# Performance work log

Hardware: AMD Instinct MI355X
Metric: run time of the kernel (lower is better)

The kernel has to match this reference:

```python
import jax, jax.numpy as jnp
import numpy as np
from jax import lax


def setup_inputs() -> dict:
    key = jax.random.key(0)
    ks = jax.random.split(key, 16)
    B, H, W, C = 4, 48, 48, 512
    N = H * W
    std = 0.02  # trunc_normal std in the torch init

    def nrm(k, shape, s=std):
        return jax.random.normal(k, shape, dtype=jnp.float32) * s

    return {
        "x": jax.random.normal(ks[0], (B, N, C), jnp.float32),
        "context": jax.random.normal(ks[1], (B, N, C), jnp.float32),
        "mask1": jax.random.uniform(ks[2], (B, N), jnp.float32),
        "mask2": jax.random.uniform(ks[3], (B, N), jnp.float32),
        "q_w": nrm(ks[4], (C, C)), "q_b": jnp.zeros((C,), jnp.float32),
        "kv1_w": nrm(ks[5], (C, C)), "kv1_b": jnp.zeros((C,), jnp.float32),
        "kv2_w": nrm(ks[6], (C, C)), "kv2_b": jnp.zeros((C,), jnp.float32),
        "f1_w": nrm(ks[7], (1, 48)), "f1_b": jnp.zeros((1,), jnp.float32),
        "f2_w": nrm(ks[8], (1, 12)), "f2_b": jnp.zeros((1,), jnp.float32),
        "lepe_w": nrm(ks[9], (C, C)), "lepe_b": jnp.zeros((C,), jnp.float32),
        "lepe_conv_w": nrm(ks[10], (C, 1, 3, 3), float(np.sqrt(2.0 / 9.0))),
        "lepe_conv_b": jnp.zeros((C,), jnp.float32),
        "proj_w": nrm(ks[11], (C, C)), "proj_b": jnp.zeros((C,), jnp.float32),
        "H": H, "W": W,
    }


def _lin(t, w, b):
    # torch nn.Linear: y = t @ W^T + b, W:[out,in]
    return t @ w.T + b


def _pooled_seq(ctx, idx, f1_w, f1_b, f2_w, f2_b):
    # ctx:[B,HW,C], idx:[B,HW] mask-sorted indices. sr_ratio==4 => groups of 48/12/1.
    B, HW, Cc = ctx.shape
    t1, t2 = HW // 192, HW // 24  # token1=(HW//48)//4, token2=(HW//12)//2
    g = jnp.take_along_axis(ctx, idx[:, :, None], axis=1)  # [B,HW,C] gathered
    p1 = g[:, : HW // 4].transpose(0, 2, 1).reshape(B, Cc, t1, 48)
    p2 = g[:, HW // 4 : 3 * HW // 4].transpose(0, 2, 1).reshape(B, Cc, t2, 12)
    p3 = g[:, 3 * HW // 4 :].transpose(0, 2, 1)  # [B,C,HW//4]
    a1 = (p1 @ f1_w.T)[..., 0] + f1_b  # [B,C,t1]
    a2 = (p2 @ f2_w.T)[..., 0] + f2_b  # [B,C,t2]
    return jnp.concatenate([a1, a2, p3], axis=-1).transpose(0, 2, 1)  # [B,Lkv,C]


def reference(x, context, mask1, mask2, q_w, q_b, kv1_w, kv1_b, kv2_w, kv2_b,
              f1_w, f1_b, f2_w, f2_b, lepe_w, lepe_b, lepe_conv_w, lepe_conv_b,
              proj_w, proj_b, H, W):
    B, N, C = x.shape
    nh = 8
    hd = C // nh
    scale = hd ** -0.5

    # lepe: linear + depthwise 3x3 conv positional encoding
    le = _lin(x, lepe_w, lepe_b).transpose(0, 2, 1).reshape(B, C, H, W)
    le = lax.conv_general_dilated(le, lepe_conv_w, (1, 1), ((1, 1), (1, 1)),
                                  dimension_numbers=("NCHW", "OIHW", "NCHW"),
                                  feature_group_count=C)
    lepe = (le + lepe_conv_b[None, :, None, None]).reshape(B, C, N).transpose(0, 2, 1)

    # mask-sorted grouped pooling of context (two orderings: row-major and transposed)
    idx1 = jnp.argsort(mask1, axis=1)
    idx2 = jnp.argsort(mask2, axis=1)
    ctx_t = context.reshape(B, H, W, C).transpose(0, 2, 1, 3).reshape(B, N, C)
    seq1 = _pooled_seq(context, idx1, f1_w, f1_b, f2_w, f2_b)
    seq2 = _pooled_seq(ctx_t, idx2, f1_w, f1_b, f2_w, f2_b)

    q = _lin(x, q_w, q_b).reshape(B, N, nh, hd).transpose(0, 2, 1, 3)  # [B,h,N,hd]
    kv1 = _lin(seq1, kv1_w, kv1_b).reshape(B, -1, 2, nh // 2, hd).transpose(2, 0, 3, 1, 4)
    kv2 = _lin(seq2, kv2_w, kv2_b).reshape(B, -1, 2, nh // 2, hd).transpose(2, 0, 3, 1, 4)
    k = jnp.concatenate([kv1[0], kv2[0]], axis=1)  # [B,h,Lkv,hd]
    v = jnp.concatenate([kv1[1], kv2[1]], axis=1)

    attn = jax.nn.softmax(jnp.einsum("bhnd,bhld->bhnl", q, k) * scale, axis=-1)
    out = jnp.einsum("bhnl,bhld->bhnd", attn, v).transpose(0, 2, 1, 3).reshape(B, N, C)
    return _lin(out + lepe, proj_w, proj_b)
```

## Files before the change

### kernel.cpp

```cpp
#include <hip/hip_runtime.h>
#include <hip/hip_bf16.h>
#include <math.h>

#define B_    4
#define H_    48
#define W_    48
#define N_    2304
#define C_    512
#define NH_   8
#define HD_   64
#define LKV_  684
#define LKP_  704

typedef __attribute__((ext_vector_type(8))) short short8;
typedef __attribute__((ext_vector_type(8))) unsigned short ushort8;
typedef __attribute__((ext_vector_type(4))) float f32x4;

#define MFMA16(a, b, c) __builtin_amdgcn_mfma_f32_16x16x32_bf16(a, b, c, 0, 0, 0)

__device__ __forceinline__ unsigned short f2bf(float f) {
  __hip_bfloat16 h = __float2bfloat16(f);
  return *reinterpret_cast<unsigned short*>(&h);
}
__device__ __forceinline__ float bf2f(unsigned short u) {
  unsigned int x = ((unsigned int)u) << 16;
  return *reinterpret_cast<float*>(&x);
}
__device__ __forceinline__ unsigned int cvtpk(float lo, float hi) {
  unsigned int r;
  asm("v_cvt_pk_bf16_f32 %0, %1, %2" : "=v"(r) : "v"(lo), "v"(hi));
  return r;
}
__device__ __forceinline__ void gld16(const unsigned short* g, unsigned short* l) {
  __builtin_amdgcn_global_load_lds(
      (const __attribute__((address_space(1))) void*)g,
      (__attribute__((address_space(3))) void*)l, 16, 0, 0);
}

#define SORTB 288
#define PACKB 1472

__global__ __launch_bounds__(256) void pack_sort(
    const float* __restrict__ lepe_w, const float* __restrict__ q_w,
    const float* __restrict__ kv1_w, const float* __restrict__ kv2_w,
    const float* __restrict__ proj_w, const float* __restrict__ x,
    unsigned short* __restrict__ wb, unsigned short* __restrict__ xb,
    const float* __restrict__ m1, const float* __restrict__ m2,
    int* __restrict__ i1, int* __restrict__ i2)
{
  __shared__ float key[N_];
  if (blockIdx.x >= SORTB) {
    int i = ((blockIdx.x - SORTB) * 256 + threadIdx.x) * 16;
    const float* s; unsigned short* d; int rel;
    if      (i < 262144)  { s = lepe_w; d = wb;           rel = i; }
    else if (i < 524288)  { s = q_w;    d = wb + 262144;  rel = i - 262144; }
    else if (i < 786432)  { s = kv1_w;  d = wb + 524288;  rel = i - 524288; }
    else if (i < 1048576) { s = kv2_w;  d = wb + 786432;  rel = i - 786432; }
    else if (i < 1310720) { s = proj_w; d = wb + 1048576; rel = i - 1048576; }
    else                  { s = x;      d = xb;           rel = i - 1310720; }
    const float4* sp = (const float4*)(s + rel);
    float4 v0 = sp[0], v1 = sp[1], v2 = sp[2], v3 = sp[3];
    ushort8 o0, o1;
    o0[0] = f2bf(v0.x); o0[1] = f2bf(v0.y); o0[2] = f2bf(v0.z); o0[3] = f2bf(v0.w);
    o0[4] = f2bf(v1.x); o0[5] = f2bf(v1.y); o0[6] = f2bf(v1.z); o0[7] = f2bf(v1.w);
    o1[0] = f2bf(v2.x); o1[1] = f2bf(v2.y); o1[2] = f2bf(v2.z); o1[3] = f2bf(v2.w);
    o1[4] = f2bf(v3.x); o1[5] = f2bf(v3.y); o1[6] = f2bf(v3.z); o1[7] = f2bf(v3.w);
    *(ushort8*)(d + rel)     = o0;
    *(ushort8*)(d + rel + 8) = o1;
    return;
  }
  const int blk = blockIdx.x;
  const int row = blk / 36, chunk = blk % 36;
  const float* m = (row < 4) ? (m1 + (size_t)row * N_) : (m2 + (size_t)(row - 4) * N_);
  int* out = (row < 4) ? (i1 + (size_t)row * N_) : (i2 + (size_t)(row - 4) * N_);
  for (int i = threadIdx.x; i < N_ / 4; i += 256)
    ((float4*)key)[i] = ((const float4*)m)[i];
  __syncthreads();
  const int e = chunk * 64 + (threadIdx.x >> 2);
  const int sl = threadIdx.x & 3;
  const float ki = key[e];
  int rank = 0;
  #pragma unroll 4
  for (int t = 0; t < N_ / 16; ++t) {
    int jb = sl * 4 + t * 16;
    float4 kv = *(const float4*)&key[jb];
    rank += (kv.x < ki) || (kv.x == ki && jb     < e);
    rank += (kv.y < ki) || (kv.y == ki && jb + 1 < e);
    rank += (kv.z < ki) || (kv.z == ki && jb + 2 < e);
    rank += (kv.w < ki) || (kv.w == ki && jb + 3 < e);
  }
  rank += __shfl_xor(rank, 1);
  rank += __shfl_xor(rank, 2);
  if (sl == 0) out[rank] = e;
}

struct GQuad {
  const unsigned short *A[4], *Bw[4];
  const float *bias[4];
  void *out[4];
  float sc[4];
  int bf[4];
  int nx[4];
  int cum[3];
};

__global__ __launch_bounds__(256) void gemm4(GQuad q, int K, int Nn)
{
  int id = blockIdx.x, cfg;
  if      (id < q.cum[0]) { cfg = 0; }
  else if (id < q.cum[1]) { cfg = 1; id -= q.cum[0]; }
  else if (id < q.cum[2]) { cfg = 2; id -= q.cum[1]; }
  else                    { cfg = 3; id -= q.cum[2]; }
  const int bx = id % q.nx[cfg], by = id / q.nx[cfg];

  const unsigned short* A  = q.A[cfg];
  const unsigned short* Bw = q.Bw[cfg];
  const float* bias        = q.bias[cfg];
  void* out                = q.out[cfg];
  const int out_bf16       = q.bf[cfg];
  const float oscale       = q.sc[cfg];

  __shared__ unsigned short Abuf[128 * 32];
  __shared__ unsigned short Bbuf[128 * 32];
  const int tid = threadIdx.x;
  const int l = tid & 63, w = tid >> 6;
  const int wm = w >> 1, wn = w & 1;
  const int lo16 = l & 15, hi = l >> 4;
  const int row0 = bx * 128, col0 = by * 128;
  const int srow = tid >> 2, scol = (tid & 3) * 8;

  const unsigned short* Asrc = A + (size_t)(row0 + srow) * K + scol;
  const unsigned short* Bsrc = Bw + (size_t)(col0 + srow) * K + scol;

  f32x4 acc[4][4];
  #pragma unroll
  for (int m = 0; m < 4; ++m)
    #pragma unroll
    for (int n = 0; n < 4; ++n)
      #pragma unroll
      for (int r = 0; r < 4; ++r) acc[m][n][r] = 0.f;

  for (int k0 = 0; k0 < K; k0 += 32) {
    __syncthreads();
    gld16(Asrc + k0,                   &Abuf[tid * 8]);
    gld16(Asrc + (size_t)64 * K + k0,  &Abuf[2048 + tid * 8]);
    gld16(Bsrc + k0,                   &Bbuf[tid * 8]);
    gld16(Bsrc + (size_t)64 * K + k0,  &Bbuf[2048 + tid * 8]);
    __syncthreads();
    short8 af[4], bf[4];
    #pragma unroll
    for (int m = 0; m < 4; ++m)
      af[m] = *(const short8*)&Abuf[(wm * 64 + m * 16 + lo16) * 32 + hi * 8];
    #pragma unroll
    for (int n = 0; n < 4; ++n)
      bf[n] = *(const short8*)&Bbuf[(wn * 64 + n * 16 + lo16) * 32 + hi * 8];
    #pragma unroll
    for (int m = 0; m < 4; ++m)
      #pragma unroll
      for (int n = 0; n < 4; ++n)
        acc[m][n] = MFMA16(af[m], bf[n], acc[m][n]);
  }

  #pragma unroll
  for (int m = 0; m < 4; ++m) {
    #pragma unroll
    for (int n = 0; n < 4; ++n) {
      int gcol = col0 + wn * 64 + n * 16 + lo16;
      #pragma unroll
      for (int r = 0; r < 4; ++r) {
        int grow = row0 + wm * 64 + m * 16 + hi * 4 + r;
        float v = acc[m][n][r] + bias[gcol];
        if (out_bf16)
          ((unsigned short*)out)[(size_t)grow * Nn + gcol] = f2bf(v * oscale);
        else
          ((float*)out)[(size_t)grow * Nn + gcol] = v;
      }
    }
  }
}

__global__ __launch_bounds__(256) void packconv(
    const unsigned short* __restrict__ kv1, const unsigned short* __restrict__ kv2,
    unsigned short* __restrict__ Kf, unsigned short* __restrict__ Vf,
    const unsigned short* __restrict__ lin, const float* __restrict__ cw,
    const float* __restrict__ cb, unsigned short* __restrict__ outp)
{
  __shared__ unsigned short Vt[64][72];
  const int tid = threadIdx.x;
  if (blockIdx.x < 352) {
    const int kb = blockIdx.x;
    const int bh = kb / 11, t = kb % 11;
    const int h = bh & 7, b = bh >> 3;
    const unsigned short* src = (h < 4) ? kv1 : kv2;
    const int hcol = (h & 3) * 64;

    #pragma unroll
    for (int pass = 0; pass < 2; ++pass) {
      int r = pass * 32 + (tid >> 3);
      int cc = (tid & 7) * 8;
      int l = t * 64 + r;
      uint4 v = make_uint4(0, 0, 0, 0);
      if (l < LKV_)
        v = *(const uint4*)&src[(size_t)(b * LKP_ + l) * C_ + 256 + hcol + cc];
      *(uint4*)&Vt[r][cc] = v;
    }
    __syncthreads();

    #pragma unroll
    for (int pass = 0; pass < 2; ++pass) {
      int o = pass * 256 + tid;
      int lane = o & 63, ns = o >> 6;
      int frag = ns >> 1, s = ns & 1;
      int lo16 = lane & 15, hi8 = (lane >> 4) * 8;
      size_t oidx = ((size_t)kb * 8 + ns) * 512 + lane * 8;
      {
        int l = t * 64 + frag * 16 + lo16;
        uint4 val = make_uint4(0, 0, 0, 0);
        if (l < LKV_)
          val = *(const uint4*)&src[(size_t)(b * LKP_ + l) * C_ + hcol + s * 32 + hi8];
        *(uint4*)&Kf[oidx] = val;
      }
      {
        unsigned short tmp[8];
        #pragma unroll
        for (int j = 0; j < 8; ++j)
          tmp[j] = Vt[s * 32 + hi8 + j][frag * 16 + lo16];
        *(uint4*)&Vf[oidx] = *(uint4*)tmp;
      }
    }
    return;
  }
  const int cg = tid & 63;
  const int wslot = (blockIdx.x - 352) * 4 + (tid >> 6);
  const int nslots = (gridDim.x - 352) * 4;

  float wf[72];
  const float* wsrc = cw + cg * 72;
  #pragma unroll
  for (int i = 0; i < 18; ++i)
    *(float4*)&wf[i * 4] = *(const float4*)(wsrc + i * 4);
  float bias[8];
  *(float4*)&bias[0] = *(const float4*)(cb + cg * 8);
  *(float4*)&bias[4] = *(const float4*)(cb + cg * 8 + 4);

  for (int pos = wslot; pos < B_ * N_; pos += nslots) {
    int wv = pos % W_;
    int r  = pos / W_;
    int hv = r % H_;
    int b  = r / H_;
    float acc[8];
    #pragma unroll
    for (int j = 0; j < 8; ++j) acc[j] = bias[j];
    #pragma unroll
    for (int dy = 0; dy < 3; ++dy) {
      int hh = hv + dy - 1;
      if (hh < 0 || hh >= H_) continue;
      #pragma unroll
      for (int dx = 0; dx < 3; ++dx) {
        int ww = wv + dx - 1;
        if (ww < 0 || ww >= W_) continue;
        ushort8 v = *(const ushort8*)(lin + ((((size_t)b * H_ + hh) * W_ + ww) * 64 + cg) * 8);
        #pragma unroll
        for (int j = 0; j < 8; ++j)
          acc[j] += wf[j * 9 + dy * 3 + dx] * bf2f(v[j]);
      }
    }
    ushort8 ov;
    #pragma unroll
    for (int j = 0; j < 8; ++j) ov[j] = f2bf(acc[j]);
    *(ushort8*)(outp + ((size_t)pos * 64 + cg) * 8) = ov;
  }
}

__global__ __launch_bounds__(256) void pool_kernel(
    const float* __restrict__ ctx,
    const int* __restrict__ idx1, const int* __restrict__ idx2,
    const float* __restrict__ f1w, const float* __restrict__ f1b,
    const float* __restrict__ f2w, const float* __restrict__ f2b_,
    unsigned short* __restrict__ seqb1, unsigned short* __restrict__ seqb2)
{
  int bl = blockIdx.x;
  const int transposed = bl >= B_ * LKP_;
  if (transposed) bl -= B_ * LKP_;
  const int* idx = transposed ? idx2 : idx1;
  unsigned short* seqb = transposed ? seqb2 : seqb1;
  int b = bl / LKP_, l = bl % LKP_;
  unsigned short* dst = seqb + ((size_t)b * LKP_ + l) * C_;
  int c0 = threadIdx.x, c1 = threadIdx.x + 256;
  if (l >= LKV_) { dst[c0] = 0; dst[c1] = 0; return; }
  const int* id = idx + (size_t)b * N_;
  int j0, cnt;
  const float* fw; float fb;
  if (l < 12)       { j0 = l * 48;              cnt = 48; fw = f1w; fb = f1b[0]; }
  else if (l < 108) { j0 = 576 + (l - 12) * 12; cnt = 12; fw = f2w; fb = f2b_[0]; }
  else              { j0 = 1728 + (l - 108);    cnt = 1;  fw = nullptr; fb = 0.f; }
  const float* cb = ctx + (size_t)b * N_ * C_;
  float a0 = fb, a1 = fb;
  int r = 0;
  for (; r + 4 <= cnt; r += 4) {
    int4 nv = *(const int4*)(id + j0 + r);
    int n0 = nv.x, n1 = nv.y, n2 = nv.z, n3 = nv.w;
    if (transposed) {
      n0 = (n0 % 48) * 48 + n0 / 48; n1 = (n1 % 48) * 48 + n1 / 48;
      n2 = (n2 % 48) * 48 + n2 / 48; n3 = (n3 % 48) * 48 + n3 / 48;
    }
    const float* s0 = cb + (size_t)n0 * C_;
    const float* s1 = cb + (size_t)n1 * C_;
    const float* s2 = cb + (size_t)n2 * C_;
    const float* s3 = cb + (size_t)n3 * C_;
    float w0 = fw[r], w1 = fw[r+1], w2 = fw[r+2], w3 = fw[r+3];
    a0 += w0 * s0[c0] + w1 * s1[c0] + w2 * s2[c0] + w3 * s3[c0];
    a1 += w0 * s0[c1] + w1 * s1[c1] + w2 * s2[c1] + w3 * s3[c1];
  }
  for (; r < cnt; ++r) {
    int n = id[j0 + r];
    if (transposed) n = (n % 48) * 48 + n / 48;
    const float* src = cb + (size_t)n * C_;
    float wr = fw ? fw[r] : 1.f;
    a0 += wr * src[c0];
    a1 += wr * src[c1];
  }
  dst[c0] = f2bf(a0);
  dst[c1] = f2bf(a1);
}

__global__ __launch_bounds__(256) void attn_kernel(
    const unsigned short* __restrict__ Qb, const unsigned short* __restrict__ Kf,
    const unsigned short* __restrict__ Vf, const unsigned short* __restrict__ lepe,
    unsigned short* __restrict__ outb)
{
  __shared__ unsigned short P[4][16][72];
  const int tid = threadIdx.x;
  const int l = tid & 63, wv = tid >> 6;
  const int lo16 = l & 15, hi = l >> 4;
  const int qt64 = blockIdx.x % (N_ / 64);
  const int bh = blockIdx.x / (N_ / 64);
  const int h = bh & 7, b = bh >> 3;
  const int qrow0 = qt64 * 64 + wv * 16;

  const unsigned short* qptr = Qb + ((size_t)b * N_ + qrow0 + lo16) * C_ + h * 64;
  short8 qf0 = *(const short8*)(qptr + hi * 8);
  short8 qf1 = *(const short8*)(qptr + 32 + hi * 8);

  const unsigned short* kbase = Kf + (size_t)bh * 11 * 4096 + (size_t)l * 8;
  const unsigned short* vbase = Vf + (size_t)bh * 11 * 4096 + (size_t)l * 8;

  float lsum = 0.f;
  f32x4 o[4];
  #pragma unroll
  for (int df = 0; df < 4; ++df)
    #pragma unroll
    for (int r = 0; r < 4; ++r) o[df][r] = 0.f;

  short8 ka0[4], ka1[4], kn0[4], kn1[4];
  #pragma unroll
  for (int n = 0; n < 4; ++n) {
    ka0[n] = *(const short8*)(kbase + (size_t)(n * 2 + 0) * 512);
    ka1[n] = *(const short8*)(kbase + (size_t)(n * 2 + 1) * 512);
  }

  for (int t = 0; t < 11; ++t) {
    short8 vf0[4], vf1[4];
    #pragma unroll
    for (int i = 0; i < 4; ++i) {
      vf0[i] = *(const short8*)(vbase + (size_t)(t * 8 + i * 2 + 0) * 512);
      vf1[i] = *(const short8*)(vbase + (size_t)(t * 8 + i * 2 + 1) * 512);
    }
    if (t < 10) {
      #pragma unroll
      for (int n = 0; n < 4; ++n) {
        kn0[n] = *(const short8*)(kbase + (size_t)((t + 1) * 8 + n * 2 + 0) * 512);
        kn1[n] = *(const short8*)(kbase + (size_t)((t + 1) * 8 + n * 2 + 1) * 512);
      }
    }
    const f32x4 z = {0.f, 0.f, 0.f, 0.f};
    f32x4 s[4];
    #pragma unroll
    for (int n = 0; n < 4; ++n) {
      s[n] = MFMA16(ka0[n], qf0, z);
      s[n] = MFMA16(ka1[n], qf1, s[n]);
    }
    if (t == 10) {
      #pragma unroll
      for (int n = 0; n < 4; ++n)
        #pragma unroll
        for (int r = 0; r < 4; ++r)
          if (n * 16 + hi * 4 + r >= LKV_ - 640) s[n][r] = -1e30f;
    }
    float psl = 0.f;
    #pragma unroll
    for (int n = 0; n < 4; ++n) {
      #pragma unroll
      for (int rp = 0; rp < 2; ++rp) {
        float e0 = exp2f(s[n][2 * rp]     - 8.f);
        float e1 = exp2f(s[n][2 * rp + 1] - 8.f);
        psl += e0 + e1;
        *(unsigned int*)&P[wv][lo16][n * 16 + hi * 4 + 2 * rp] = cvtpk(e0, e1);
      }
    }
    lsum += psl;
    short8 pa0 = *(const short8*)&P[wv][lo16][hi * 8];
    short8 pa1 = *(const short8*)&P[wv][lo16][32 + hi * 8];
    #pragma unroll
    for (int df = 0; df < 4; ++df) {
      o[df] = MFMA16(pa0, vf0[df], o[df]);
      o[df] = MFMA16(pa1, vf1[df], o[df]);
    }
    #pragma unroll
    for (int n = 0; n < 4; ++n) { ka0[n] = kn0[n]; ka1[n] = kn1[n]; }
  }

  lsum += __shfl_xor(lsum, 16);
  lsum += __shfl_xor(lsum, 32);
  float rr[4];
  #pragma unroll
  for (int r = 0; r < 4; ++r) rr[r] = 1.f / __shfl(lsum, hi * 4 + r);
  #pragma unroll
  for (int df = 0; df < 4; ++df)
    #pragma unroll
    for (int r = 0; r < 4; ++r) {
      size_t off = ((size_t)b * N_ + qrow0 + hi * 4 + r) * C_ + h * 64 + df * 16 + lo16;
      outb[off] = f2bf(o[df][r] * rr[r] + bf2f(lepe[off]));
    }
}

extern "C" void kernel_launch(void* const* d_in, const int* in_sizes, int n_in,
                              void* d_out, int out_size, void* d_ws, size_t ws_size,
                              hipStream_t stream)
{
  const float* x      = (const float*)d_in[0];
  const float* ctx    = (const float*)d_in[1];
  const float* mask1  = (const float*)d_in[2];
  const float* mask2  = (const float*)d_in[3];
  const float* q_w    = (const float*)d_in[4];
  const float* q_b    = (const float*)d_in[5];
  const float* kv1_w  = (const float*)d_in[6];
  const float* kv1_b  = (const float*)d_in[7];
  const float* kv2_w  = (const float*)d_in[8];
  const float* kv2_b  = (const float*)d_in[9];
  const float* f1_w   = (const float*)d_in[10];
  const float* f1_b   = (const float*)d_in[11];
  const float* f2_w   = (const float*)d_in[12];
  const float* f2_b   = (const float*)d_in[13];
  const float* lepe_w = (const float*)d_in[14];
  const float* lepe_b = (const float*)d_in[15];
  const float* lcw    = (const float*)d_in[16];
  const float* lcb    = (const float*)d_in[17];
  const float* proj_w = (const float*)d_in[18];
  const float* proj_b = (const float*)d_in[19];
  float* outp = (float*)d_out;

  char* ws = (char*)d_ws;
  unsigned short* bufA  = (unsigned short*)(ws);
  unsigned short* bufB  = (unsigned short*)(ws + 18874368);
  unsigned short* xb    = (unsigned short*)(ws + 37748736);
  unsigned short* Qb    = (unsigned short*)(ws + 47185920);
  unsigned short* wb    = (unsigned short*)(ws + 56623104);
  unsigned short* seqb1 = (unsigned short*)(ws + 59244544);
  unsigned short* seqb2 = (unsigned short*)(ws + 62128128);
  unsigned short* kv1b  = (unsigned short*)(ws + 65011712);
  unsigned short* kv2b  = (unsigned short*)(ws + 67895296);
  unsigned short* Kf    = (unsigned short*)(ws + 70778880);
  unsigned short* Vf    = (unsigned short*)(ws + 73662464);
  int*            idx1  = (int*)(ws + 76546048);
  int*            idx2  = (int*)(ws + 76582912);

  unsigned short* wb_lepe = wb;
  unsigned short* wb_q    = wb + 262144;
  unsigned short* wb_kv1  = wb + 524288;
  unsigned short* wb_kv2  = wb + 786432;
  unsigned short* wb_proj = wb + 1048576;

  dim3 blk(256);

  pack_sort<<<dim3(SORTB + PACKB), blk, 0, stream>>>(
      lepe_w, q_w, kv1_w, kv2_w, proj_w, x, wb, xb, mask1, mask2, idx1, idx2);

  pool_kernel<<<dim3(2 * B_ * LKP_), blk, 0, stream>>>(
      ctx, idx1, idx2, f1_w, f1_b, f2_w, f2_b, seqb1, seqb2);

  {
    GQuad q;
    q.A[0] = seqb1; q.Bw[0] = wb_kv1;  q.bias[0] = kv1_b;  q.out[0] = (void*)kv1b;
    q.A[1] = seqb2; q.Bw[1] = wb_kv2;  q.bias[1] = kv2_b;  q.out[1] = (void*)kv2b;
    q.A[2] = xb;    q.Bw[2] = wb_lepe; q.bias[2] = lepe_b; q.out[2] = (void*)bufA;
    q.A[3] = xb;    q.Bw[3] = wb_q;    q.bias[3] = q_b;    q.out[3] = (void*)Qb;
    q.sc[0] = 1.f; q.sc[1] = 1.f; q.sc[2] = 1.f; q.sc[3] = 0.18033688011112042f;
    q.bf[0] = 1; q.bf[1] = 1; q.bf[2] = 1; q.bf[3] = 1;
    q.nx[0] = 22; q.nx[1] = 22; q.nx[2] = 72; q.nx[3] = 72;
    q.cum[0] = 88; q.cum[1] = 176; q.cum[2] = 464;
    gemm4<<<dim3(752), blk, 0, stream>>>(q, C_, C_);
  }

  packconv<<<dim3(736), blk, 0, stream>>>(kv1b, kv2b, Kf, Vf, bufA, lcw, lcb, bufB);

  attn_kernel<<<dim3(B_ * NH_ * (N_ / 64)), blk, 0, stream>>>(Qb, Kf, Vf, bufB, xb);

  {
    GQuad q;
    q.A[0] = xb; q.Bw[0] = wb_proj; q.bias[0] = proj_b; q.out[0] = (void*)outp;
    q.A[1] = q.A[2] = q.A[3] = xb;
    q.Bw[1] = q.Bw[2] = q.Bw[3] = wb_proj;
    q.bias[1] = q.bias[2] = q.bias[3] = proj_b;
    q.out[1] = q.out[2] = q.out[3] = (void*)outp;
    q.sc[0] = q.sc[1] = q.sc[2] = q.sc[3] = 1.f;
    q.bf[0] = q.bf[1] = q.bf[2] = q.bf[3] = 0;
    q.nx[0] = q.nx[1] = q.nx[2] = q.nx[3] = 72;
    q.cum[0] = q.cum[1] = q.cum[2] = 288;
    gemm4<<<dim3(288), blk, 0, stream>>>(q, C_, C_);
  }
}
```

Before: 149.1 us.

## Split KV tiles across two wave groups in attention and merge partials via LDS

```diff
diff --git a/kernel.cpp b/kernel.cpp
--- a/kernel.cpp
+++ b/kernel.cpp
@@ -324,19 +324,22 @@
   dst[c1] = f2bf(a1);
 }
 
-__global__ __launch_bounds__(256) void attn_kernel(
+__global__ __launch_bounds__(512) void attn_kernel(
     const unsigned short* __restrict__ Qb, const unsigned short* __restrict__ Kf,
     const unsigned short* __restrict__ Vf, const unsigned short* __restrict__ lepe,
     unsigned short* __restrict__ outb)
 {
-  __shared__ unsigned short P[4][16][72];
+  __shared__ unsigned short P[8][16][72];
+  __shared__ float Ob[4][16][68];
+  __shared__ float Ls[4][16];
   const int tid = threadIdx.x;
   const int l = tid & 63, wv = tid >> 6;
+  const int pair = wv & 3, half = wv >> 2;
   const int lo16 = l & 15, hi = l >> 4;
   const int qt64 = blockIdx.x % (N_ / 64);
   const int bh = blockIdx.x / (N_ / 64);
   const int h = bh & 7, b = bh >> 3;
-  const int qrow0 = qt64 * 64 + wv * 16;
+  const int qrow0 = qt64 * 64 + pair * 16;
 
   const unsigned short* qptr = Qb + ((size_t)b * N_ + qrow0 + lo16) * C_ + h * 64;
   short8 qf0 = *(const short8*)(qptr + hi * 8);
@@ -344,6 +347,9 @@
 
   const unsigned short* kbase = Kf + (size_t)bh * 11 * 4096 + (size_t)l * 8;
   const unsigned short* vbase = Vf + (size_t)bh * 11 * 4096 + (size_t)l * 8;
+
+  const int tstart = half ? 6 : 0;
+  const int tend   = half ? 11 : 6;
 
   float lsum = 0.f;
   f32x4 o[4];
@@ -355,18 +361,18 @@
   short8 ka0[4], ka1[4], kn0[4], kn1[4];
   #pragma unroll
   for (int n = 0; n < 4; ++n) {
-    ka0[n] = *(const short8*)(kbase + (size_t)(n * 2 + 0) * 512);
-    ka1[n] = *(const short8*)(kbase + (size_t)(n * 2 + 1) * 512);
-  }
-
-  for (int t = 0; t < 11; ++t) {
+    ka0[n] = *(const short8*)(kbase + (size_t)(tstart * 8 + n * 2 + 0) * 512);
+    ka1[n] = *(const short8*)(kbase + (size_t)(tstart * 8 + n * 2 + 1) * 512);
+  }
+
+  for (int t = tstart; t < tend; ++t) {
     short8 vf0[4], vf1[4];
     #pragma unroll
     for (int i = 0; i < 4; ++i) {
       vf0[i] = *(const short8*)(vbase + (size_t)(t * 8 + i * 2 + 0) * 512);
       vf1[i] = *(const short8*)(vbase + (size_t)(t * 8 + i * 2 + 1) * 512);
     }
-    if (t < 10) {
+    if (t + 1 < tend) {
       #pragma unroll
       for (int n = 0; n < 4; ++n) {
         kn0[n] = *(const short8*)(kbase + (size_t)((t + 1) * 8 + n * 2 + 0) * 512);
@@ -412,16 +418,30 @@
 
   lsum += __shfl_xor(lsum, 16);
   lsum += __shfl_xor(lsum, 32);
-  float rr[4];
-  #pragma unroll
-  for (int r = 0; r < 4; ++r) rr[r] = 1.f / __shfl(lsum, hi * 4 + r);
-  #pragma unroll
-  for (int df = 0; df < 4; ++df)
-    #pragma unroll
-    for (int r = 0; r < 4; ++r) {
-      size_t off = ((size_t)b * N_ + qrow0 + hi * 4 + r) * C_ + h * 64 + df * 16 + lo16;
-      outb[off] = f2bf(o[df][r] * rr[r] + bf2f(lepe[off]));
-    }
+
+  if (half) {
+    #pragma unroll
+    for (int df = 0; df < 4; ++df)
+      #pragma unroll
+      for (int r = 0; r < 4; ++r)
+        Ob[pair][hi * 4 + r][df * 16 + lo16] = o[df][r];
+    if (hi == 0) Ls[pair][lo16] = lsum;
+  }
+  __syncthreads();
+  if (!half) {
+    float lt = lsum + Ls[pair][lo16];
+    float rr[4];
+    #pragma unroll
+    for (int r = 0; r < 4; ++r) rr[r] = 1.f / __shfl(lt, hi * 4 + r);
+    #pragma unroll
+    for (int df = 0; df < 4; ++df)
+      #pragma unroll
+      for (int r = 0; r < 4; ++r) {
+        float ov = o[df][r] + Ob[pair][hi * 4 + r][df * 16 + lo16];
+        size_t off = ((size_t)b * N_ + qrow0 + hi * 4 + r) * C_ + h * 64 + df * 16 + lo16;
+        outb[off] = f2bf(ov * rr[r] + bf2f(lepe[off]));
+      }
+  }
 }
 
 extern "C" void kernel_launch(void* const* d_in, const int* in_sizes, int n_in,
@@ -494,7 +514,7 @@
 
   packconv<<<dim3(736), blk, 0, stream>>>(kv1b, kv2b, Kf, Vf, bufA, lcw, lcb, bufB);
 
-  attn_kernel<<<dim3(B_ * NH_ * (N_ / 64)), blk, 0, stream>>>(Qb, Kf, Vf, bufB, xb);
+  attn_kernel<<<dim3(B_ * NH_ * (N_ / 64)), dim3(512), 0, stream>>>(Qb, Kf, Vf, bufB, xb);
 
   {
     GQuad q;
```

Result: slower. 155.0 us (+3.9%).
